# Optimization experiments

Hardware: AMD Instinct MI355X
Metric: run time of the kernel (lower is better)

The kernel has to match this reference:

```python
import jax, jax.numpy as jnp
import numpy as np

N = 20000
E = 320000
HID = 256
NUM_RBF = 32
CUTOFF = 6.0
NUM_EDGE_TYPES = 2
LIGAND_NODE = 1
EPS = 1e-5

CENTERS = jnp.linspace(0.0, CUTOFF, NUM_RBF)  # [R]
GAMMA = 1.0 / max(float(CENTERS[1] - CENTERS[0]) ** 2, 1e-6)


def setup_inputs() -> dict:
    key = jax.random.key(0)
    ks = jax.random.split(key, 16)
    d = {}
    d['h'] = jax.random.normal(ks[0], (N, HID), dtype=jnp.float32)
    d['pos'] = jax.random.normal(ks[1], (N, 3), dtype=jnp.float32)
    d['edge_index'] = jax.random.randint(ks[2], (2, E), 0, N)
    d['edge_type'] = jax.random.randint(ks[3], (E,), 0, NUM_EDGE_TYPES)
    d['node_type'] = jax.random.randint(ks[4], (N,), 0, 2)
    s_in = 1.0 / np.sqrt(3 * HID + NUM_RBF)
    s_h = 1.0 / np.sqrt(HID)
    s_2h = 1.0 / np.sqrt(2 * HID)
    d['emb'] = jax.random.normal(ks[5], (NUM_EDGE_TYPES, HID), dtype=jnp.float32)
    d['W1m'] = jax.random.normal(ks[6], (3 * HID + NUM_RBF, HID), dtype=jnp.float32) * s_in
    d['b1m'] = jnp.zeros((HID,), dtype=jnp.float32)
    d['W2m'] = jax.random.normal(ks[7], (HID, HID), dtype=jnp.float32) * s_h
    d['b2m'] = jnp.zeros((HID,), dtype=jnp.float32)
    d['W1u'] = jax.random.normal(ks[8], (2 * HID, HID), dtype=jnp.float32) * s_2h
    d['b1u'] = jnp.zeros((HID,), dtype=jnp.float32)
    d['W2u'] = jax.random.normal(ks[9], (HID, HID), dtype=jnp.float32) * s_h
    d['b2u'] = jnp.zeros((HID,), dtype=jnp.float32)
    d['ln_g'] = jnp.ones((HID,), dtype=jnp.float32)
    d['ln_b'] = jnp.zeros((HID,), dtype=jnp.float32)
    return d


def _layernorm(x, g, b):
    mu = jnp.mean(x, axis=-1, keepdims=True)
    var = jnp.mean(jnp.square(x - mu), axis=-1, keepdims=True)
    return (x - mu) * jax.lax.rsqrt(var + EPS) * g + b


def reference(h, pos, edge_index, edge_type, node_type,
              emb, W1m, b1m, W2m, b2m, W1u, b1u, W2u, b2u, ln_g, ln_b):
    src, dst = edge_index[0], edge_index[1]
    rel = pos[src] - pos[dst]                      # [E,3]
    dist = jnp.linalg.norm(rel, axis=-1)           # [E]
    radial = jnp.exp(-GAMMA * jnp.square(dist[:, None] - CENTERS[None, :]))  # [E,R]
    edge_kind = emb[edge_type]                     # [E,H]
    m_in = jnp.concatenate([h[src], h[dst], edge_kind, radial], axis=-1)  # [E,3H+R]
    m = jax.nn.silu(m_in @ W1m + b1m)
    m_ij = jax.nn.silu(m @ W2m + b2m)              # [E,H] (dropout = identity in eval)
    seg_sum = jax.ops.segment_sum(m_ij, dst, num_segments=N)               # [N,H]
    cnt = jax.ops.segment_sum(jnp.ones((m_ij.shape[0],), m_ij.dtype), dst, num_segments=N)
    m_i = seg_sum / jnp.maximum(cnt, 1.0)[:, None]
    u = jax.nn.silu(jnp.concatenate([h, m_i], axis=-1) @ W1u + b1u)
    upd = u @ W2u + b2u                            # [N,H]
    lig = (node_type == LIGAND_NODE)[:, None]
    out = jnp.where(lig, _layernorm(h + upd, ln_g, ln_b), h)
    return out
```

## Files before the change

kernel.cpp:

```cpp
#include <hip/hip_runtime.h>
#include <hip/hip_fp16.h>
#include <math.h>

#define NN   20000
#define EE   320000
#define HID  256
#define GAMMA_C ((31.0f/6.0f)*(31.0f/6.0f))

typedef __attribute__((ext_vector_type(8)))  short    short8;
typedef __attribute__((ext_vector_type(8)))  _Float16 half8;
typedef __attribute__((ext_vector_type(16))) float    f32x16;

__device__ __forceinline__ float silu_f(float x) {
    return x / (1.0f + __expf(-x));
}

__device__ __forceinline__ short bf_hi(float x) {
    unsigned u = __float_as_uint(x);
    return (short)((u + 0x7fffu + ((u >> 16) & 1u)) >> 16);
}
__device__ __forceinline__ float bf_tof(short b) {
    return __uint_as_float(((unsigned)(unsigned short)b) << 16);
}
__device__ __forceinline__ void cvt_bf16_pair(float x, short* hi, short* lo) {
    short h = bf_hi(x);
    *hi = h;
    *lo = bf_hi(x - bf_tof(h));
}
__device__ __forceinline__ void cvt_f16_pair(float x, short* hi, short* lo) {
    __half h = __float2half_rn(x);
    *hi = (short)__half_as_ushort(h);
    *lo = (short)__half_as_ushort(__float2half_rn(x - __half2float(h)));
}
__device__ __forceinline__ short f16_bits(float x) {
    return (short)__half_as_ushort(__float2half_rn(x));
}

typedef __attribute__((address_space(1))) const void GV;
typedef __attribute__((address_space(3))) void LV;
__device__ __forceinline__ void gll16(const void* g, void* l) {
    __builtin_amdgcn_global_load_lds((GV*)g, (LV*)l, 16, 0, 0);
}

__device__ __forceinline__ short8 ldsfrag(const short* t, int row, int sg) {
    int s = sg ^ (row & 7);
    return *(const short8*)&t[row * 64 + s * 8];
}
__device__ __forceinline__ half8 ldsfragh32(const short* t, int row, int sg) {
    int s = sg ^ (row & 3);
    return *(const half8*)&t[row * 32 + s * 8];
}
__device__ __forceinline__ short8 ldsfrag32(const short* t, int row, int sg) {
    int s = sg ^ (row & 3);
    return *(const short8*)&t[row * 32 + s * 8];
}
__device__ __forceinline__ half8 ldsfragh(const short* t, int row, int sg) {
    int s = sg ^ (row & 7);
    return *(const half8*)&t[row * 64 + s * 8];
}

#define S0 (NN*HID)
#define S1 (2*HID)
#define S2 (256*800)
#define S3 (256*256)
#define S4 (256*512)
#define S5 (256*256)
#define PREP_TOTAL (S0+S1+S2+S3+S4+S5)

__global__ __launch_bounds__(256) void prep_all(
    const float* __restrict__ h, const float* __restrict__ emb,
    const float* __restrict__ W1m, const float* __restrict__ W2m,
    const float* __restrict__ W1u, const float* __restrict__ W2u,
    short* __restrict__ hpl, short* __restrict__ embpl,
    short* __restrict__ w1t, short* __restrict__ w2t,
    short* __restrict__ w1ut, short* __restrict__ w2ut)
{
    int i = blockIdx.x * 256 + threadIdx.x;
    float x; short *hi, *lo; int o; int f16 = 0;
    if (i < S0)              { x = h[i];   hi = hpl;   lo = hpl + S0;   o = i; }
    else if ((i -= S0) < S1) { x = emb[i]; hi = embpl; lo = embpl + S1; o = i; }
    else if ((i -= S1) < S2) { int n = i / 800, k = i - n * 800;
                               x = W1m[k * 256 + n]; hi = w1t; lo = w1t + S2; o = i; }
    else if ((i -= S2) < S3) { int n = i >> 8, k = i & 255;
                               x = W2m[k * 256 + n]; hi = w2t; lo = w2t + S3; o = i; f16 = 1; }
    else if ((i -= S3) < S4) { int n = i >> 9, k = i & 511;
                               x = W1u[k * 256 + n]; hi = w1ut; lo = w1ut + S4; o = i; }
    else if ((i -= S4) < S5) { int n = i >> 8, k = i & 255;
                               x = W2u[k * 256 + n]; hi = w2ut; lo = w2ut + S5; o = i; f16 = 1; }
    else return;
    short hb, lb;
    if (f16) cvt_f16_pair(x, &hb, &lb); else cvt_bf16_pair(x, &hb, &lb);
    hi[o] = hb; lo[o] = lb;
}

__global__ __launch_bounds__(512, 4) void edge_mlp1(
    const short* __restrict__ hpl, const short* __restrict__ embpl,
    const short* __restrict__ w1t, const float* __restrict__ b1,
    const float* __restrict__ pos, const int* __restrict__ ei,
    const int* __restrict__ etype,
    short* __restrict__ mhi, float* __restrict__ cnt)
{
    __shared__ __align__(16) short At[2][128 * 64];
    __shared__ __align__(16) short Bt[2][128 * 64];
    __shared__ int srcS[128], dstS[128], etS[128];
    __shared__ float distS[128];

    const int tid = threadIdx.x, l = tid & 63, w = tid >> 6;
    const int e0 = blockIdx.x * 128;
    const int cb = blockIdx.y;
    const int mh = w >> 2, ns = w & 3;

    if (tid < 128) {
        int s = ei[e0 + tid], d = ei[EE + e0 + tid];
        srcS[tid] = s; dstS[tid] = d; etS[tid] = etype[e0 + tid];
        float dx = pos[3*s]   - pos[3*d];
        float dy = pos[3*s+1] - pos[3*d+1];
        float dz = pos[3*s+2] - pos[3*d+2];
        distS[tid] = sqrtf(dx*dx + dy*dy + dz*dz);
        if (cb == 0) atomicAdd(&cnt[d], 1.0f);
    }
    __syncthreads();

    auto stageA = [&](int buf, int c) {
        if (c < 24) {
            #pragma unroll
            for (int jj = 0; jj < 2; ++jj) {
                int j = w * 2 + jj;
                int row = j * 8 + (l >> 3), s = l & 7;
                int sg = s ^ (row & 7);
                int hl = sg >> 2, q = sg & 3;
                const short* gp;
                if (c < 8)
                    gp = hpl + (size_t)hl * (NN*HID) + (size_t)srcS[row] * HID + c*32 + q*8;
                else if (c < 16)
                    gp = hpl + (size_t)hl * (NN*HID) + (size_t)dstS[row] * HID + (c-8)*32 + q*8;
                else
                    gp = embpl + hl * (2*HID) + etS[row] * HID + (c-16)*32 + q*8;
                gll16(gp, &At[buf][j * 512]);
            }
        } else {
            #pragma unroll
            for (int jj = 0; jj < 2; ++jj) {
                int it = tid * 2 + jj;
                int row = it >> 3, s = it & 7;
                int sg = s ^ (row & 7);
                int hl = sg >> 2, q = sg & 3;
                float d = distS[row];
                short8 v;
                #pragma unroll
                for (int k8 = 0; k8 < 8; ++k8) {
                    float cen = (float)(q * 8 + k8) * (6.0f / 31.0f);
                    float t = d - cen;
                    float f = __expf(-GAMMA_C * t * t);
                    short hb = bf_hi(f);
                    v[k8] = hl ? bf_hi(f - bf_tof(hb)) : hb;
                }
                *(short8*)&At[buf][row * 64 + s * 8] = v;
            }
        }
    };
    auto stageB = [&](int buf, int c) {
        #pragma unroll
        for (int jj = 0; jj < 2; ++jj) {
            int j = w * 2 + jj;
            int n = j * 8 + (l >> 3), s = l & 7;
            int sg = s ^ (n & 7);
            int hl = sg >> 2, q = sg & 3;
            const short* gp = w1t + (size_t)hl * (256*800)
                            + (size_t)(cb*128 + n) * 800 + c*32 + q*8;
            gll16(gp, &Bt[buf][j * 512]);
        }
    };

    f32x16 acc[2];
    #pragma unroll
    for (int a = 0; a < 2; ++a)
        #pragma unroll
        for (int q = 0; q < 16; ++q) acc[a][q] = 0.0f;

    stageA(0, 0); stageB(0, 0);
    __syncthreads();

    int cur = 0;
    for (int c = 0; c < 25; ++c) {
        if (c < 24) { stageA(cur ^ 1, c + 1); stageB(cur ^ 1, c + 1); }
        #pragma unroll
        for (int t2 = 0; t2 < 2; ++t2) {
            short8 aF[2][2], bF[2];
            #pragma unroll
            for (int mf = 0; mf < 2; ++mf) {
                int row = mh * 64 + mf * 32 + (l & 31);
                #pragma unroll
                for (int hl = 0; hl < 2; ++hl)
                    aF[mf][hl] = ldsfrag(&At[cur][0], row, hl * 4 + t2 * 2 + (l >> 5));
            }
            {
                int n = ns * 32 + (l & 31);
                #pragma unroll
                for (int hl = 0; hl < 2; ++hl)
                    bF[hl] = ldsfrag(&Bt[cur][0], n, hl * 4 + t2 * 2 + (l >> 5));
            }
            #pragma unroll
            for (int mf = 0; mf < 2; ++mf) {
                acc[mf] = __builtin_amdgcn_mfma_f32_32x32x16_bf16(aF[mf][0], bF[0], acc[mf], 0, 0, 0);
                acc[mf] = __builtin_amdgcn_mfma_f32_32x32x16_bf16(aF[mf][0], bF[1], acc[mf], 0, 0, 0);
                acc[mf] = __builtin_amdgcn_mfma_f32_32x32x16_bf16(aF[mf][1], bF[0], acc[mf], 0, 0, 0);
            }
        }
        __syncthreads();
        cur ^= 1;
    }

    {
        int col = cb * 128 + ns * 32 + (l & 31);
        float bb = b1[col];
        #pragma unroll
        for (int mf = 0; mf < 2; ++mf)
            #pragma unroll
            for (int r = 0; r < 16; ++r) {
                int row = mh * 64 + mf * 32 + (r & 3) + 8 * (r >> 2) + 4 * (l >> 5);
                float v = silu_f(acc[mf][r] + bb);
                mhi[(size_t)(e0 + row) * HID + col] = f16_bits(v);
            }
    }
}

__global__ __launch_bounds__(512, 4) void edge_mlp2(
    const short* __restrict__ mhi, const short* __restrict__ w2t,
    const float* __restrict__ b2, const int* __restrict__ ei,
    float* __restrict__ seg)
{
    __shared__ __align__(16) short Ah[2][128 * 32];
    __shared__ __align__(16) short Bh[2][128 * 32];
    __shared__ __align__(16) short Bl[2][128 * 32];
    __shared__ int dstS[128];
    const int tid = threadIdx.x, l = tid & 63, w = tid >> 6;
    const int e0 = blockIdx.x * 128;
    const int cb = blockIdx.y;
    const int mh = w >> 2, ns = w & 3;
    if (tid < 128) dstS[tid] = ei[EE + e0 + tid];
    __syncthreads();

    auto stageA = [&](int buf, int c) {
        int row = w * 16 + (l >> 2), s = l & 3;
        int sg = s ^ (row & 3);
        gll16(mhi + (size_t)(e0 + row) * HID + c * 32 + sg * 8, &Ah[buf][w * 512]);
    };
    auto stageB = [&](int buf, int c) {
        #pragma unroll
        for (int jj = 0; jj < 2; ++jj) {
            int j = w * 2 + jj;
            int hf = j >> 3, jn = j & 7;
            int n = jn * 16 + (l >> 2), s = l & 3;
            int sg = s ^ (n & 3);
            const short* gp = w2t + (size_t)hf * (256*256)
                            + (size_t)(cb*128 + n) * HID + c * 32 + sg * 8;
            gll16(gp, hf ? &Bl[buf][jn * 512] : &Bh[buf][jn * 512]);
        }
    };

    f32x16 acc[2];
    #pragma unroll
    for (int a = 0; a < 2; ++a)
        #pragma unroll
        for (int q = 0; q < 16; ++q) acc[a][q] = 0.0f;

    stageA(0, 0); stageB(0, 0);
    __syncthreads();

    int cur = 0;
    for (int c = 0; c < 8; ++c) {
        if (c < 7) { stageA(cur ^ 1, c + 1); stageB(cur ^ 1, c + 1); }
        #pragma unroll
        for (int t2 = 0; t2 < 2; ++t2) {
            int sg = t2 * 2 + (l >> 5);
            half8 aF[2], bH, bL;
            #pragma unroll
            for (int mf = 0; mf < 2; ++mf)
                aF[mf] = ldsfragh32(&Ah[cur][0], mh * 64 + mf * 32 + (l & 31), sg);
            {
                int n = ns * 32 + (l & 31);
                bH = ldsfragh32(&Bh[cur][0], n, sg);
                bL = ldsfragh32(&Bl[cur][0], n, sg);
            }
            #pragma unroll
            for (int mf = 0; mf < 2; ++mf) {
                acc[mf] = __builtin_amdgcn_mfma_f32_32x32x16_f16(aF[mf], bH, acc[mf], 0, 0, 0);
                acc[mf] = __builtin_amdgcn_mfma_f32_32x32x16_f16(aF[mf], bL, acc[mf], 0, 0, 0);
            }
        }
        __syncthreads();
        cur ^= 1;
    }

    {
        int col = cb * 128 + ns * 32 + (l & 31);
        float bb = b2[col];
        #pragma unroll
        for (int mf = 0; mf < 2; ++mf)
            #pragma unroll
            for (int r = 0; r < 16; ++r) {
                int row = mh * 64 + mf * 32 + (r & 3) + 8 * (r >> 2) + 4 * (l >> 5);
                float v = silu_f(acc[mf][r] + bb);
                atomicAdd(&seg[(size_t)dstS[row] * HID + col], v);
            }
    }
}

__global__ __launch_bounds__(256) void mi_prep(
    const float* __restrict__ seg, const float* __restrict__ cnt,
    short* __restrict__ mipl)
{
    int i = blockIdx.x * 256 + threadIdx.x;
    int row = i >> 8;
    float v = seg[i] / fmaxf(cnt[row], 1.0f);
    short hb, lb;
    cvt_bf16_pair(v, &hb, &lb);
    mipl[i] = hb;
    mipl[(size_t)NN * HID + i] = lb;
}

__global__ __launch_bounds__(512) void node_mlp1(
    const short* __restrict__ hpl, const short* __restrict__ mipl,
    const short* __restrict__ w1ut, const float* __restrict__ b1,
    short* __restrict__ u)
{
    __shared__ __align__(16) short At[128 * 64];
    __shared__ __align__(16) short Bt[256 * 64];
    const int tid = threadIdx.x, l = tid & 63, w = tid >> 6;
    const int n0 = blockIdx.x * 128;
    const int mh = w >> 2, ns = w & 3;

    f32x16 acc[2][2];
    #pragma unroll
    for (int a = 0; a < 2; ++a)
        #pragma unroll
        for (int b = 0; b < 2; ++b)
            #pragma unroll
            for (int q = 0; q < 16; ++q) acc[a][b][q] = 0.0f;

    for (int c = 0; c < 16; ++c) {
        #pragma unroll
        for (int jj = 0; jj < 2; ++jj) {
            int j = w * 2 + jj;
            int row = j * 8 + (l >> 3), s = l & 7;
            int sg = s ^ (row & 7);
            int hl = sg >> 2, q = sg & 3;
            int node = min(n0 + row, NN - 1);
            const short* gp = (c < 8)
                ? hpl  + (size_t)hl * (NN*HID) + (size_t)node * HID + c * 32 + q * 8
                : mipl + (size_t)hl * (NN*HID) + (size_t)node * HID + (c - 8) * 32 + q * 8;
            gll16(gp, &At[j * 512]);
        }
        #pragma unroll
        for (int jj = 0; jj < 4; ++jj) {
            int j = w * 4 + jj;
            int n = j * 8 + (l >> 3), s = l & 7;
            int sg = s ^ (n & 7);
            int hl = sg >> 2, q = sg & 3;
            const short* gp = w1ut + (size_t)hl * (256*512) + n * 512 + c * 32 + q * 8;
            gll16(gp, &Bt[j * 512]);
        }
        __syncthreads();
        #pragma unroll
        for (int t2 = 0; t2 < 2; ++t2) {
            short8 aF[2][2], bF[2][2];
            #pragma unroll
            for (int mf = 0; mf < 2; ++mf) {
                int row = mh * 64 + mf * 32 + (l & 31);
                #pragma unroll
                for (int hl = 0; hl < 2; ++hl)
                    aF[mf][hl] = ldsfrag(At, row, hl * 4 + t2 * 2 + (l >> 5));
            }
            #pragma unroll
            for (int nf = 0; nf < 2; ++nf) {
                int n = ns * 64 + nf * 32 + (l & 31);
                #pragma unroll
                for (int hl = 0; hl < 2; ++hl)
                    bF[nf][hl] = ldsfrag(Bt, n, hl * 4 + t2 * 2 + (l >> 5));
            }
            #pragma unroll
            for (int mf = 0; mf < 2; ++mf)
                #pragma unroll
                for (int nf = 0; nf < 2; ++nf) {
                    acc[mf][nf] = __builtin_amdgcn_mfma_f32_32x32x16_bf16(aF[mf][0], bF[nf][0], acc[mf][nf], 0, 0, 0);
                    acc[mf][nf] = __builtin_amdgcn_mfma_f32_32x32x16_bf16(aF[mf][0], bF[nf][1], acc[mf][nf], 0, 0, 0);
                    acc[mf][nf] = __builtin_amdgcn_mfma_f32_32x32x16_bf16(aF[mf][1], bF[nf][0], acc[mf][nf], 0, 0, 0);
                }
        }
        __syncthreads();
    }
    #pragma unroll
    for (int nf = 0; nf < 2; ++nf) {
        int col = ns * 64 + nf * 32 + (l & 31);
        float bb = b1[col];
        #pragma unroll
        for (int mf = 0; mf < 2; ++mf)
            #pragma unroll
            for (int r = 0; r < 16; ++r) {
                int row = mh * 64 + mf * 32 + (r & 3) + 8 * (r >> 2) + 4 * (l >> 5);
                if (n0 + row < NN) {
                    float v = silu_f(acc[mf][nf][r] + bb);
                    u[(size_t)(n0 + row) * HID + col] = f16_bits(v);
                }
            }
    }
}

__global__ __launch_bounds__(512) void node_mlp2(
    const short* __restrict__ u, const short* __restrict__ w2ut,
    const float* __restrict__ b2, const float* __restrict__ h,
    const int* __restrict__ ntype, const float* __restrict__ lng,
    const float* __restrict__ lnb, float* __restrict__ out)
{
    __shared__ __align__(16) short Ah[128 * 64];
    __shared__ __align__(16) short Bh[256 * 64];
    __shared__ __align__(16) short Bl[256 * 64];
    __shared__ float red1[4][128], red2[4][128];
    __shared__ float muS[128], rsS[128];
    const int tid = threadIdx.x, l = tid & 63, w = tid >> 6;
    const int n0 = blockIdx.x * 128;
    const int mh = w >> 2, ns = w & 3;

    f32x16 acc[2][2];
    #pragma unroll
    for (int a = 0; a < 2; ++a)
        #pragma unroll
        for (int b = 0; b < 2; ++b)
            #pragma unroll
            for (int q = 0; q < 16; ++q) acc[a][b][q] = 0.0f;

    for (int c = 0; c < 4; ++c) {
        #pragma unroll
        for (int jj = 0; jj < 2; ++jj) {
            int j = w * 2 + jj;
            int row = j * 8 + (l >> 3), s = l & 7;
            int sg = s ^ (row & 7);
            int node = min(n0 + row, NN - 1);
            gll16(u + (size_t)node * HID + c * 64 + sg * 8, &Ah[j * 512]);
        }
        #pragma unroll
        for (int jj = 0; jj < 8; ++jj) {
            int j = w * 8 + jj;
            int hf = j >> 5;
            int n = (j & 31) * 8 + (l >> 3), s = l & 7;
            int sg = s ^ (n & 7);
            const short* gp = w2ut + (size_t)hf * (256*256) + n * HID + c * 64 + sg * 8;
            gll16(gp, hf ? &Bl[(j & 31) * 512] : &Bh[(j & 31) * 512]);
        }
        __syncthreads();
        #pragma unroll
        for (int t2 = 0; t2 < 4; ++t2) {
            int sg = t2 * 2 + (l >> 5);
            half8 aF[2], bH[2], bL[2];
            #pragma unroll
            for (int mf = 0; mf < 2; ++mf)
                aF[mf] = ldsfragh(Ah, mh * 64 + mf * 32 + (l & 31), sg);
            #pragma unroll
            for (int nf = 0; nf < 2; ++nf) {
                int n = ns * 64 + nf * 32 + (l & 31);
                bH[nf] = ldsfragh(Bh, n, sg);
                bL[nf] = ldsfragh(Bl, n, sg);
            }
            #pragma unroll
            for (int mf = 0; mf < 2; ++mf)
                #pragma unroll
                for (int nf = 0; nf < 2; ++nf) {
                    acc[mf][nf] = __builtin_amdgcn_mfma_f32_32x32x16_f16(aF[mf], bH[nf], acc[mf][nf], 0, 0, 0);
                    acc[mf][nf] = __builtin_amdgcn_mfma_f32_32x32x16_f16(aF[mf], bL[nf], acc[mf][nf], 0, 0, 0);
                }
        }
        __syncthreads();
    }

    #pragma unroll
    for (int nf = 0; nf < 2; ++nf) {
        int col = ns * 64 + nf * 32 + (l & 31);
        float bb = b2[col];
        #pragma unroll
        for (int mf = 0; mf < 2; ++mf)
            #pragma unroll
            for (int r = 0; r < 16; ++r) {
                int row = mh * 64 + mf * 32 + (r & 3) + 8 * (r >> 2) + 4 * (l >> 5);
                int node = min(n0 + row, NN - 1);
                acc[mf][nf][r] += bb + h[(size_t)node * HID + col];
            }
    }
    #pragma unroll
    for (int mf = 0; mf < 2; ++mf)
        #pragma unroll
        for (int r = 0; r < 16; ++r) {
            float v1 = acc[mf][0][r] + acc[mf][1][r];
            float v2 = acc[mf][0][r]*acc[mf][0][r] + acc[mf][1][r]*acc[mf][1][r];
            #pragma unroll
            for (int off = 16; off >= 1; off >>= 1) {
                v1 += __shfl_xor(v1, off, 64);
                v2 += __shfl_xor(v2, off, 64);
            }
            if ((l & 31) == 0) {
                int row = mh * 64 + mf * 32 + (r & 3) + 8 * (r >> 2) + 4 * (l >> 5);
                red1[ns][row] = v1; red2[ns][row] = v2;
            }
        }
    __syncthreads();
    if (tid < 128) {
        float s1 = red1[0][tid] + red1[1][tid] + red1[2][tid] + red1[3][tid];
        float s2 = red2[0][tid] + red2[1][tid] + red2[2][tid] + red2[3][tid];
        float mu = s1 * (1.0f / 256.0f);
        float var = s2 * (1.0f / 256.0f) - mu * mu;
        muS[tid] = mu;
        rsS[tid] = rsqrtf(var + 1e-5f);
    }
    __syncthreads();
    #pragma unroll
    for (int nf = 0; nf < 2; ++nf) {
        int col = ns * 64 + nf * 32 + (l & 31);
        float g = lng[col], bt = lnb[col];
        #pragma unroll
        for (int mf = 0; mf < 2; ++mf)
            #pragma unroll
            for (int r = 0; r < 16; ++r) {
                int row = mh * 64 + mf * 32 + (r & 3) + 8 * (r >> 2) + 4 * (l >> 5);
                int node = n0 + row;
                if (node < NN) {
                    float y;
                    if (ntype[node] == 1)
                        y = (acc[mf][nf][r] - muS[row]) * rsS[row] * g + bt;
                    else
                        y = h[(size_t)node * HID + col];
                    out[(size_t)node * HID + col] = y;
                }
            }
    }
}

#define SWZ(k, e) ((e) ^ ((((k) >> 2) & 7) << 2))

__global__ __launch_bounds__(256) void edge_fp32(
    const float* __restrict__ h, const float* __restrict__ pos,
    const int* __restrict__ ei, const int* __restrict__ etype,
    const float* __restrict__ emb,
    const float* __restrict__ W1, const float* __restrict__ b1,
    const float* __restrict__ W2, const float* __restrict__ b2,
    float* __restrict__ seg, float* __restrict__ cnt)
{
    __shared__ float A1T[16][32];
    __shared__ float Bt[16][256];
    __shared__ float A2T[256][32];
    __shared__ float distS[32];
    __shared__ int   srcS[32], dstS[32], etS[32];
    const int tid = threadIdx.x;
    const int e0  = blockIdx.x * 32;
    if (tid < 32) {
        const int e = e0 + tid;
        const int s = ei[e];
        const int d = ei[EE + e];
        srcS[tid] = s; dstS[tid] = d; etS[tid] = etype[e];
        const float dx = pos[3*s+0] - pos[3*d+0];
        const float dy = pos[3*s+1] - pos[3*d+1];
        const float dz = pos[3*s+2] - pos[3*d+2];
        distS[tid] = sqrtf(dx*dx + dy*dy + dz*dz);
        atomicAdd(&cnt[d], 1.0f);
    }
    __syncthreads();
    const int c0 = (tid & 63) * 4;
    const int r0 = (tid >> 6) * 8;
    float acc[8][4];
    #pragma unroll
    for (int i = 0; i < 8; ++i)
        #pragma unroll
        for (int j = 0; j < 4; ++j) acc[i][j] = 0.0f;
    const float step  = 6.0f / 31.0f;
    for (int k0 = 0; k0 < 800; k0 += 16) {
        if (tid < 128) {
            const int e = tid >> 2;
            const int q = (tid & 3) * 4;
            const int k = k0 + q;
            float4 v;
            if (k < 256)       v = *(const float4*)&h[(size_t)srcS[e]*HID + k];
            else if (k < 512)  v = *(const float4*)&h[(size_t)dstS[e]*HID + (k - 256)];
            else if (k < 768)  v = *(const float4*)&emb[(size_t)etS[e]*HID + (k - 512)];
            else {
                const float de = distS[e];
                const float t0 = de - step*(float)(k-768);
                const float t1 = de - step*(float)(k-767);
                const float t2 = de - step*(float)(k-766);
                const float t3 = de - step*(float)(k-765);
                v = make_float4(__expf(-GAMMA_C*t0*t0), __expf(-GAMMA_C*t1*t1),
                                __expf(-GAMMA_C*t2*t2), __expf(-GAMMA_C*t3*t3));
            }
            A1T[q+0][e] = v.x; A1T[q+1][e] = v.y;
            A1T[q+2][e] = v.z; A1T[q+3][e] = v.w;
        }
        #pragma unroll
        for (int p = 0; p < 4; ++p) {
            const int idx = p*256 + tid;
            const int k   = idx >> 6;
            const int n   = (idx & 63) * 4;
            *(float4*)&Bt[k][n] = *(const float4*)&W1[(size_t)(k0+k)*HID + n];
        }
        __syncthreads();
        #pragma unroll
        for (int kk = 0; kk < 16; ++kk) {
            const float4 b  = *(const float4*)&Bt[kk][c0];
            const float4 a0 = *(const float4*)&A1T[kk][r0];
            const float4 a1 = *(const float4*)&A1T[kk][r0+4];
            const float a[8] = {a0.x,a0.y,a0.z,a0.w,a1.x,a1.y,a1.z,a1.w};
            #pragma unroll
            for (int i = 0; i < 8; ++i) {
                acc[i][0] = fmaf(a[i], b.x, acc[i][0]);
                acc[i][1] = fmaf(a[i], b.y, acc[i][1]);
                acc[i][2] = fmaf(a[i], b.z, acc[i][2]);
                acc[i][3] = fmaf(a[i], b.w, acc[i][3]);
            }
        }
        __syncthreads();
    }
    {
        const float4 b1v = *(const float4*)&b1[c0];
        const float bb[4] = {b1v.x, b1v.y, b1v.z, b1v.w};
        #pragma unroll
        for (int j = 0; j < 4; ++j) {
            const int k = c0 + j;
            #pragma unroll
            for (int i = 0; i < 8; ++i) {
                const float x = acc[i][j] + bb[j];
                A2T[k][SWZ(k, r0+i)] = silu_f(x);
                acc[i][j] = 0.0f;
            }
        }
    }
    __syncthreads();
    for (int k0 = 0; k0 < HID; k0 += 16) {
        #pragma unroll
        for (int p = 0; p < 4; ++p) {
            const int idx = p*256 + tid;
            const int k   = idx >> 6;
            const int n   = (idx & 63) * 4;
            *(float4*)&Bt[k][n] = *(const float4*)&W2[(size_t)(k0+k)*HID + n];
        }
        __syncthreads();
        #pragma unroll
        for (int kk = 0; kk < 16; ++kk) {
            const int K = k0 + kk;
            const float4 b  = *(const float4*)&Bt[kk][c0];
            const float4 a0 = *(const float4*)&A2T[K][SWZ(K, r0)];
            const float4 a1 = *(const float4*)&A2T[K][SWZ(K, r0+4)];
            const float a[8] = {a0.x,a0.y,a0.z,a0.w,a1.x,a1.y,a1.z,a1.w};
            #pragma unroll
            for (int i = 0; i < 8; ++i) {
                acc[i][0] = fmaf(a[i], b.x, acc[i][0]);
                acc[i][1] = fmaf(a[i], b.y, acc[i][1]);
                acc[i][2] = fmaf(a[i], b.z, acc[i][2]);
                acc[i][3] = fmaf(a[i], b.w, acc[i][3]);
            }
        }
        __syncthreads();
    }
    {
        const float4 b2v = *(const float4*)&b2[c0];
        const float bb[4] = {b2v.x, b2v.y, b2v.z, b2v.w};
        #pragma unroll
        for (int i = 0; i < 8; ++i) {
            const int d = dstS[r0 + i];
            float* outp = &seg[(size_t)d*HID + c0];
            #pragma unroll
            for (int j = 0; j < 4; ++j) {
                const float x = acc[i][j] + bb[j];
                atomicAdd(&outp[j], silu_f(x));
            }
        }
    }
}

__global__ __launch_bounds__(256) void node_fp32(
    const float* __restrict__ h, const float* __restrict__ seg,
    const float* __restrict__ cnt, const int* __restrict__ ntype,
    const float* __restrict__ W1, const float* __restrict__ b1,
    const float* __restrict__ W2, const float* __restrict__ b2,
    const float* __restrict__ lng, const float* __restrict__ lnb,
    float* __restrict__ out)
{
    __shared__ float A1T[16][32];
    __shared__ float Bt[16][256];
    __shared__ float A2T[256][32];
    __shared__ float invS[32];
    const int tid = threadIdx.x;
    const int n0  = blockIdx.x * 32;
    if (tid < 32) invS[tid] = 1.0f / fmaxf(cnt[n0 + tid], 1.0f);
    __syncthreads();
    const int c0 = (tid & 63) * 4;
    const int r0 = (tid >> 6) * 8;
    float acc[8][4];
    #pragma unroll
    for (int i = 0; i < 8; ++i)
        #pragma unroll
        for (int j = 0; j < 4; ++j) acc[i][j] = 0.0f;
    for (int k0 = 0; k0 < 512; k0 += 16) {
        if (tid < 128) {
            const int e = tid >> 2;
            const int q = (tid & 3) * 4;
            const int k = k0 + q;
            float4 v;
            if (k < 256) v = *(const float4*)&h[(size_t)(n0+e)*HID + k];
            else {
                v = *(const float4*)&seg[(size_t)(n0+e)*HID + (k - 256)];
                const float ic = invS[e];
                v.x *= ic; v.y *= ic; v.z *= ic; v.w *= ic;
            }
            A1T[q+0][e] = v.x; A1T[q+1][e] = v.y;
            A1T[q+2][e] = v.z; A1T[q+3][e] = v.w;
        }
        #pragma unroll
        for (int p = 0; p < 4; ++p) {
            const int idx = p*256 + tid;
            const int k   = idx >> 6;
            const int n   = (idx & 63) * 4;
            *(float4*)&Bt[k][n] = *(const float4*)&W1[(size_t)(k0+k)*HID + n];
        }
        __syncthreads();
        #pragma unroll
        for (int kk = 0; kk < 16; ++kk) {
            const float4 b  = *(const float4*)&Bt[kk][c0];
            const float4 a0 = *(const float4*)&A1T[kk][r0];
            const float4 a1 = *(const float4*)&A1T[kk][r0+4];
            const float a[8] = {a0.x,a0.y,a0.z,a0.w,a1.x,a1.y,a1.z,a1.w};
            #pragma unroll
            for (int i = 0; i < 8; ++i) {
                acc[i][0] = fmaf(a[i], b.x, acc[i][0]);
                acc[i][1] = fmaf(a[i], b.y, acc[i][1]);
                acc[i][2] = fmaf(a[i], b.z, acc[i][2]);
                acc[i][3] = fmaf(a[i], b.w, acc[i][3]);
            }
        }
        __syncthreads();
    }
    {
        const float4 b1v = *(const float4*)&b1[c0];
        const float bb[4] = {b1v.x, b1v.y, b1v.z, b1v.w};
        #pragma unroll
        for (int j = 0; j < 4; ++j) {
            const int k = c0 + j;
            #pragma unroll
            for (int i = 0; i < 8; ++i) {
                const float x = acc[i][j] + bb[j];
                A2T[k][SWZ(k, r0+i)] = silu_f(x);
                acc[i][j] = 0.0f;
            }
        }
    }
    __syncthreads();
    for (int k0 = 0; k0 < HID; k0 += 16) {
        #pragma unroll
        for (int p = 0; p < 4; ++p) {
            const int idx = p*256 + tid;
            const int k   = idx >> 6;
            const int n   = (idx & 63) * 4;
            *(float4*)&Bt[k][n] = *(const float4*)&W2[(size_t)(k0+k)*HID + n];
        }
        __syncthreads();
        #pragma unroll
        for (int kk = 0; kk < 16; ++kk) {
            const int K = k0 + kk;
            const float4 b  = *(const float4*)&Bt[kk][c0];
            const float4 a0 = *(const float4*)&A2T[K][SWZ(K, r0)];
            const float4 a1 = *(const float4*)&A2T[K][SWZ(K, r0+4)];
            const float a[8] = {a0.x,a0.y,a0.z,a0.w,a1.x,a1.y,a1.z,a1.w};
            #pragma unroll
            for (int i = 0; i < 8; ++i) {
                acc[i][0] = fmaf(a[i], b.x, acc[i][0]);
                acc[i][1] = fmaf(a[i], b.y, acc[i][1]);
                acc[i][2] = fmaf(a[i], b.z, acc[i][2]);
                acc[i][3] = fmaf(a[i], b.w, acc[i][3]);
            }
        }
        __syncthreads();
    }
    {
        const float4 b2v = *(const float4*)&b2[c0];
        const float bb[4] = {b2v.x, b2v.y, b2v.z, b2v.w};
        float4 hv[8];
        #pragma unroll
        for (int i = 0; i < 8; ++i) {
            hv[i] = *(const float4*)&h[(size_t)(n0+r0+i)*HID + c0];
            acc[i][0] = hv[i].x + acc[i][0] + bb[0];
            acc[i][1] = hv[i].y + acc[i][1] + bb[1];
            acc[i][2] = hv[i].z + acc[i][2] + bb[2];
            acc[i][3] = hv[i].w + acc[i][3] + bb[3];
        }
        float s1[8], s2[8];
        #pragma unroll
        for (int i = 0; i < 8; ++i) {
            s1[i] = acc[i][0] + acc[i][1] + acc[i][2] + acc[i][3];
            s2[i] = acc[i][0]*acc[i][0] + acc[i][1]*acc[i][1]
                  + acc[i][2]*acc[i][2] + acc[i][3]*acc[i][3];
        }
        #pragma unroll
        for (int off = 32; off >= 1; off >>= 1) {
            #pragma unroll
            for (int i = 0; i < 8; ++i) {
                s1[i] += __shfl_xor(s1[i], off, 64);
                s2[i] += __shfl_xor(s2[i], off, 64);
            }
        }
        const float4 gv = *(const float4*)&lng[c0];
        const float4 bv = *(const float4*)&lnb[c0];
        const float g[4] = {gv.x, gv.y, gv.z, gv.w};
        const float bb2[4] = {bv.x, bv.y, bv.z, bv.w};
        #pragma unroll
        for (int i = 0; i < 8; ++i) {
            const int n = n0 + r0 + i;
            const bool lig = (ntype[n] == 1);
            float4 y;
            if (lig) {
                const float mu  = s1[i] * (1.0f/256.0f);
                const float var = s2[i] * (1.0f/256.0f) - mu*mu;
                const float rs  = rsqrtf(var + 1e-5f);
                y.x = (acc[i][0] - mu) * rs * g[0] + bb2[0];
                y.y = (acc[i][1] - mu) * rs * g[1] + bb2[1];
                y.z = (acc[i][2] - mu) * rs * g[2] + bb2[2];
                y.w = (acc[i][3] - mu) * rs * g[3] + bb2[3];
            } else {
                y = hv[i];
            }
            *(float4*)&out[(size_t)n*HID + c0] = y;
        }
    }
}

extern "C" void kernel_launch(void* const* d_in, const int* in_sizes, int n_in,
                              void* d_out, int out_size, void* d_ws, size_t ws_size,
                              hipStream_t stream) {
    (void)in_sizes; (void)n_in; (void)out_size;
    const float* h    = (const float*)d_in[0];
    const float* pos  = (const float*)d_in[1];
    const int*   ei   = (const int*)  d_in[2];
    const int*   et   = (const int*)  d_in[3];
    const int*   nt   = (const int*)  d_in[4];
    const float* emb  = (const float*)d_in[5];
    const float* W1m  = (const float*)d_in[6];
    const float* b1m  = (const float*)d_in[7];
    const float* W2m  = (const float*)d_in[8];
    const float* b2m  = (const float*)d_in[9];
    const float* W1u  = (const float*)d_in[10];
    const float* b1u  = (const float*)d_in[11];
    const float* W2u  = (const float*)d_in[12];
    const float* b2u  = (const float*)d_in[13];
    const float* lng  = (const float*)d_in[14];
    const float* lnb  = (const float*)d_in[15];
    float* out = (float*)d_out;

    size_t o = 0;
    auto al = [&](size_t b) { size_t r = o; o = (o + b + 511) & ~(size_t)511; return r; };
    const size_t o_seg  = al((size_t)NN * HID * 4);
    const size_t o_cnt  = al((size_t)NN * 4);
    const size_t o_zend = o;
    const size_t o_hpl  = al((size_t)2 * NN * HID * 2);
    const size_t o_emb  = al((size_t)2 * 2 * HID * 2);
    const size_t o_w1t  = al((size_t)2 * 256 * 800 * 2);
    const size_t o_w2t  = al((size_t)2 * 256 * 256 * 2);
    const size_t o_w1ut = al((size_t)2 * 256 * 512 * 2);
    const size_t o_w2ut = al((size_t)2 * 256 * 256 * 2);
    const size_t o_mipl = al((size_t)2 * NN * HID * 2);
    const size_t o_upl  = al((size_t)NN * HID * 2);
    const size_t o_mhi  = al((size_t)EE * HID * 2);
    const size_t need = o;

    char* ws = (char*)d_ws;
    float* seg = (float*)(ws + o_seg);
    float* cnt = (float*)(ws + o_cnt);

    if (ws_size >= need) {
        short* hpl   = (short*)(ws + o_hpl);
        short* embpl = (short*)(ws + o_emb);
        short* w1t   = (short*)(ws + o_w1t);
        short* w2t   = (short*)(ws + o_w2t);
        short* w1ut  = (short*)(ws + o_w1ut);
        short* w2ut  = (short*)(ws + o_w2ut);
        short* mipl  = (short*)(ws + o_mipl);
        short* upl   = (short*)(ws + o_upl);
        short* mhi   = (short*)(ws + o_mhi);

        hipMemsetAsync(d_ws, 0, o_zend, stream);
        prep_all<<<PREP_TOTAL / 256, 256, 0, stream>>>(
            h, emb, W1m, W2m, W1u, W2u, hpl, embpl, w1t, w2t, w1ut, w2ut);
        edge_mlp1<<<dim3(EE / 128, 2), 512, 0, stream>>>(
            hpl, embpl, w1t, b1m, pos, ei, et, mhi, cnt);
        edge_mlp2<<<dim3(EE / 128, 2), 512, 0, stream>>>(mhi, w2t, b2m, ei, seg);
        mi_prep<<<(NN * HID) / 256, 256, 0, stream>>>(seg, cnt, mipl);
        const int nb = (NN + 127) / 128;
        node_mlp1<<<nb, 512, 0, stream>>>(hpl, mipl, w1ut, b1u, upl);
        node_mlp2<<<nb, 512, 0, stream>>>(upl, w2ut, b2u, h, nt, lng, lnb, out);
    } else {
        hipMemsetAsync(d_ws, 0, ((size_t)NN * HID + NN) * sizeof(float), stream);
        float* seg0 = (float*)d_ws;
        float* cnt0 = seg0 + (size_t)NN * HID;
        edge_fp32<<<EE / 32, 256, 0, stream>>>(h, pos, ei, et, emb,
                                               W1m, b1m, W2m, b2m, seg0, cnt0);
        node_fp32<<<NN / 32, 256, 0, stream>>>(h, seg0, cnt0, nt,
                                               W1u, b1u, W2u, b2u, lng, lnb, out);
    }
}
```

Measured before the change: 935.8 us.

## Fold edge-type embedding into per-type bias table and enlarge edge_mlp1 tile

Since the edge-type embedding takes one of only two values, its product with W1m plus b1m is precomputed into a 2x256 table by a small kernel and added in the epilogue, which shrinks the K dimension of the first edge GEMM from 800 to 544. edge_mlp1 is also retiled to 256 edges by the full 256 output columns per block, which removes the two-column-block grid and the duplicated gathers of h rows. The mainloop becomes a hand-pipelined double buffer with explicit vmcnt waits and raw barriers. The cost is more accumulator registers and LDS per block (occupancy bound lowered to 2) and a serial single-block tprep launch.

Result: faster. 872.4 us (-6.8%).

```diff
diff --git a/kernel.cpp b/kernel.cpp
--- a/kernel.cpp
+++ b/kernel.cpp
@@ -5,6 +5,7 @@
 #define NN   20000
 #define EE   320000
 #define HID  256
+#define K1P  544
 #define GAMMA_C ((31.0f/6.0f)*(31.0f/6.0f))
 
 typedef __attribute__((ext_vector_type(8)))  short    short8;
@@ -50,10 +51,6 @@
     int s = sg ^ (row & 3);
     return *(const half8*)&t[row * 32 + s * 8];
 }
-__device__ __forceinline__ short8 ldsfrag32(const short* t, int row, int sg) {
-    int s = sg ^ (row & 3);
-    return *(const short8*)&t[row * 32 + s * 8];
-}
 __device__ __forceinline__ half8 ldsfragh(const short* t, int row, int sg) {
     int s = sg ^ (row & 7);
     return *(const half8*)&t[row * 64 + s * 8];
@@ -61,7 +58,7 @@
 
 #define S0 (NN*HID)
 #define S1 (2*HID)
-#define S2 (256*800)
+#define S2 (256*544)
 #define S3 (256*256)
 #define S4 (256*512)
 #define S5 (256*256)
@@ -79,8 +76,9 @@
     float x; short *hi, *lo; int o; int f16 = 0;
     if (i < S0)              { x = h[i];   hi = hpl;   lo = hpl + S0;   o = i; }
     else if ((i -= S0) < S1) { x = emb[i]; hi = embpl; lo = embpl + S1; o = i; }
-    else if ((i -= S1) < S2) { int n = i / 800, k = i - n * 800;
-                               x = W1m[k * 256 + n]; hi = w1t; lo = w1t + S2; o = i; }
+    else if ((i -= S1) < S2) { int n = i / 544, k = i - n * 544;
+                               int ok = (k < 512) ? k : (k + 256);
+                               x = W1m[ok * 256 + n]; hi = w1t; lo = w1t + S2; o = i; }
     else if ((i -= S2) < S3) { int n = i >> 8, k = i & 255;
                                x = W2m[k * 256 + n]; hi = w2t; lo = w2t + S3; o = i; f16 = 1; }
     else if ((i -= S3) < S4) { int n = i >> 9, k = i & 511;
@@ -93,55 +91,68 @@
     hi[o] = hb; lo[o] = lb;
 }
 
-__global__ __launch_bounds__(512, 4) void edge_mlp1(
-    const short* __restrict__ hpl, const short* __restrict__ embpl,
-    const short* __restrict__ w1t, const float* __restrict__ b1,
-    const float* __restrict__ pos, const int* __restrict__ ei,
-    const int* __restrict__ etype,
+__global__ __launch_bounds__(512) void tprep(
+    const float* __restrict__ W1m, const float* __restrict__ b1,
+    const float* __restrict__ emb, float* __restrict__ T)
+{
+    int tid = threadIdx.x;
+    int e = tid >> 8, n = tid & 255;
+    float s = b1[n];
+    for (int k = 0; k < 256; ++k)
+        s += emb[e * 256 + k] * W1m[(512 + k) * 256 + n];
+    T[e * 256 + n] = s;
+}
+
+__global__ __launch_bounds__(512, 2) void edge_mlp1(
+    const short* __restrict__ hpl, const short* __restrict__ w1t,
+    const float* __restrict__ Ttab, const float* __restrict__ pos,
+    const int* __restrict__ ei, const int* __restrict__ etype,
     short* __restrict__ mhi, float* __restrict__ cnt)
 {
-    __shared__ __align__(16) short At[2][128 * 64];
-    __shared__ __align__(16) short Bt[2][128 * 64];
-    __shared__ int srcS[128], dstS[128], etS[128];
-    __shared__ float distS[128];
+    __shared__ __align__(16) short At[2][256 * 64];
+    __shared__ __align__(16) short Bt[2][256 * 64];
+    __shared__ int srcS[256], dstS[256], etS[256];
+    __shared__ float distS[256];
 
     const int tid = threadIdx.x, l = tid & 63, w = tid >> 6;
-    const int e0 = blockIdx.x * 128;
-    const int cb = blockIdx.y;
+    const int e0 = blockIdx.x * 256;
     const int mh = w >> 2, ns = w & 3;
 
-    if (tid < 128) {
+    if (tid < 256) {
         int s = ei[e0 + tid], d = ei[EE + e0 + tid];
         srcS[tid] = s; dstS[tid] = d; etS[tid] = etype[e0 + tid];
         float dx = pos[3*s]   - pos[3*d];
         float dy = pos[3*s+1] - pos[3*d+1];
         float dz = pos[3*s+2] - pos[3*d+2];
         distS[tid] = sqrtf(dx*dx + dy*dy + dz*dz);
-        if (cb == 0) atomicAdd(&cnt[d], 1.0f);
+        atomicAdd(&cnt[d], 1.0f);
     }
     __syncthreads();
 
-    auto stageA = [&](int buf, int c) {
-        if (c < 24) {
-            #pragma unroll
-            for (int jj = 0; jj < 2; ++jj) {
-                int j = w * 2 + jj;
-                int row = j * 8 + (l >> 3), s = l & 7;
-                int sg = s ^ (row & 7);
-                int hl = sg >> 2, q = sg & 3;
-                const short* gp;
-                if (c < 8)
-                    gp = hpl + (size_t)hl * (NN*HID) + (size_t)srcS[row] * HID + c*32 + q*8;
-                else if (c < 16)
-                    gp = hpl + (size_t)hl * (NN*HID) + (size_t)dstS[row] * HID + (c-8)*32 + q*8;
-                else
-                    gp = embpl + hl * (2*HID) + etS[row] * HID + (c-16)*32 + q*8;
-                gll16(gp, &At[buf][j * 512]);
+    unsigned offS[4], offD[4], offB[4];
+    #pragma unroll
+    for (int jj = 0; jj < 4; ++jj) {
+        int j = w * 4 + jj;
+        int row = j * 8 + (l >> 3), s = l & 7;
+        int sg = s ^ (row & 7);
+        int hl = sg >> 2, q = sg & 3;
+        offS[jj] = (unsigned)hl * (NN*HID) + (unsigned)srcS[row] * HID + q*8;
+        offD[jj] = (unsigned)hl * (NN*HID) + (unsigned)dstS[row] * HID + q*8;
+        offB[jj] = (unsigned)hl * (256*544) + (unsigned)row * 544 + q*8;
+    }
+
+    auto stage = [&](int buf, int c) {
+        if (c < 16) {
+            #pragma unroll
+            for (int jj = 0; jj < 4; ++jj) {
+                const short* gp = (c < 8) ? (hpl + offS[jj] + c*32)
+                                          : (hpl + offD[jj] + (c-8)*32);
+                gll16(gp, &At[buf][(w*4 + jj) * 512]);
             }
         } else {
             #pragma unroll
-            for (int jj = 0; jj < 2; ++jj) {
-                int it = tid * 2 + jj;
+            for (int jj = 0; jj < 4; ++jj) {
+                int it = tid * 4 + jj;
                 int row = it >> 3, s = it & 7;
                 int sg = s ^ (row & 7);
                 int hl = sg >> 2, q = sg & 3;
@@ -157,69 +168,70 @@
                 }
                 *(short8*)&At[buf][row * 64 + s * 8] = v;
             }
-        }
+            asm volatile("s_waitcnt lgkmcnt(0)" ::: "memory");
+        }
+        #pragma unroll
+        for (int jj = 0; jj < 4; ++jj)
+            gll16(w1t + offB[jj] + c*32, &Bt[buf][(w*4 + jj) * 512]);
     };
-    auto stageB = [&](int buf, int c) {
-        #pragma unroll
-        for (int jj = 0; jj < 2; ++jj) {
-            int j = w * 2 + jj;
-            int n = j * 8 + (l >> 3), s = l & 7;
-            int sg = s ^ (n & 7);
-            int hl = sg >> 2, q = sg & 3;
-            const short* gp = w1t + (size_t)hl * (256*800)
-                            + (size_t)(cb*128 + n) * 800 + c*32 + q*8;
-            gll16(gp, &Bt[buf][j * 512]);
-        }
-    };
-
-    f32x16 acc[2];
-    #pragma unroll
-    for (int a = 0; a < 2; ++a)
-        #pragma unroll
-        for (int q = 0; q < 16; ++q) acc[a][q] = 0.0f;
-
-    stageA(0, 0); stageB(0, 0);
-    __syncthreads();
-
-    int cur = 0;
-    for (int c = 0; c < 25; ++c) {
-        if (c < 24) { stageA(cur ^ 1, c + 1); stageB(cur ^ 1, c + 1); }
+
+    f32x16 acc[4][2];
+    #pragma unroll
+    for (int a = 0; a < 4; ++a)
+        #pragma unroll
+        for (int b = 0; b < 2; ++b)
+            #pragma unroll
+            for (int q = 0; q < 16; ++q) acc[a][b][q] = 0.0f;
+
+    stage(0, 0);
+    stage(1, 1);
+
+    for (int c = 0; c <= 16; ++c) {
+        if (c <= 14)      asm volatile("s_waitcnt vmcnt(8)" ::: "memory");
+        else if (c == 15) asm volatile("s_waitcnt vmcnt(4)" ::: "memory");
+        else              asm volatile("s_waitcnt vmcnt(0)" ::: "memory");
+        __builtin_amdgcn_s_barrier();
+        __builtin_amdgcn_sched_barrier(0);
+
+        const int buf = c & 1;
         #pragma unroll
         for (int t2 = 0; t2 < 2; ++t2) {
-            short8 aF[2][2], bF[2];
-            #pragma unroll
-            for (int mf = 0; mf < 2; ++mf) {
-                int row = mh * 64 + mf * 32 + (l & 31);
+            short8 bF[2][2];
+            #pragma unroll
+            for (int nf = 0; nf < 2; ++nf)
                 #pragma unroll
                 for (int hl = 0; hl < 2; ++hl)
-                    aF[mf][hl] = ldsfrag(&At[cur][0], row, hl * 4 + t2 * 2 + (l >> 5));
-            }
-            {
-                int n = ns * 32 + (l & 31);
+                    bF[nf][hl] = ldsfrag(&Bt[buf][0], ns*64 + nf*32 + (l & 31),
+                                         hl*4 + t2*2 + (l >> 5));
+            #pragma unroll
+            for (int mf = 0; mf < 4; ++mf) {
+                int arow = mh*128 + mf*32 + (l & 31);
+                short8 aF0 = ldsfrag(&At[buf][0], arow, 0*4 + t2*2 + (l >> 5));
+                short8 aF1 = ldsfrag(&At[buf][0], arow, 1*4 + t2*2 + (l >> 5));
                 #pragma unroll
-                for (int hl = 0; hl < 2; ++hl)
-                    bF[hl] = ldsfrag(&Bt[cur][0], n, hl * 4 + t2 * 2 + (l >> 5));
-            }
-            #pragma unroll
-            for (int mf = 0; mf < 2; ++mf) {
-                acc[mf] = __builtin_amdgcn_mfma_f32_32x32x16_bf16(aF[mf][0], bF[0], acc[mf], 0, 0, 0);
-                acc[mf] = __builtin_amdgcn_mfma_f32_32x32x16_bf16(aF[mf][0], bF[1], acc[mf], 0, 0, 0);
-                acc[mf] = __builtin_amdgcn_mfma_f32_32x32x16_bf16(aF[mf][1], bF[0], acc[mf], 0, 0, 0);
-            }
-        }
-        __syncthreads();
-        cur ^= 1;
-    }
-
-    {
-        int col = cb * 128 + ns * 32 + (l & 31);
-        float bb = b1[col];
-        #pragma unroll
-        for (int mf = 0; mf < 2; ++mf)
+                for (int nf = 0; nf < 2; ++nf) {
+                    acc[mf][nf] = __builtin_amdgcn_mfma_f32_32x32x16_bf16(aF0, bF[nf][0], acc[mf][nf], 0, 0, 0);
+                    acc[mf][nf] = __builtin_amdgcn_mfma_f32_32x32x16_bf16(aF0, bF[nf][1], acc[mf][nf], 0, 0, 0);
+                    acc[mf][nf] = __builtin_amdgcn_mfma_f32_32x32x16_bf16(aF1, bF[nf][0], acc[mf][nf], 0, 0, 0);
+                }
+            }
+        }
+
+        __builtin_amdgcn_sched_barrier(0);
+        __builtin_amdgcn_s_barrier();
+        if (c + 2 <= 16) stage(buf, c + 2);
+    }
+
+    #pragma unroll
+    for (int nf = 0; nf < 2; ++nf) {
+        int col = ns*64 + nf*32 + (l & 31);
+        #pragma unroll
+        for (int mf = 0; mf < 4; ++mf)
             #pragma unroll
             for (int r = 0; r < 16; ++r) {
-                int row = mh * 64 + mf * 32 + (r & 3) + 8 * (r >> 2) + 4 * (l >> 5);
-                float v = silu_f(acc[mf][r] + bb);
+                int row = mh*128 + mf*32 + (r & 3) + 8*(r >> 2) + 4*(l >> 5);
+                float tv = Ttab[etS[row] * 256 + col];
+                float v = silu_f(acc[mf][nf][r] + tv);
                 mhi[(size_t)(e0 + row) * HID + col] = f16_bits(v);
             }
     }
@@ -857,10 +869,11 @@
     const size_t o_zend = o;
     const size_t o_hpl  = al((size_t)2 * NN * HID * 2);
     const size_t o_emb  = al((size_t)2 * 2 * HID * 2);
-    const size_t o_w1t  = al((size_t)2 * 256 * 800 * 2);
+    const size_t o_w1t  = al((size_t)2 * 256 * 544 * 2);
     const size_t o_w2t  = al((size_t)2 * 256 * 256 * 2);
     const size_t o_w1ut = al((size_t)2 * 256 * 512 * 2);
     const size_t o_w2ut = al((size_t)2 * 256 * 256 * 2);
+    const size_t o_T    = al((size_t)2 * 256 * 4);
     const size_t o_mipl = al((size_t)2 * NN * HID * 2);
     const size_t o_upl  = al((size_t)NN * HID * 2);
     const size_t o_mhi  = al((size_t)EE * HID * 2);
@@ -877,6 +890,7 @@
         short* w2t   = (short*)(ws + o_w2t);
         short* w1ut  = (short*)(ws + o_w1ut);
         short* w2ut  = (short*)(ws + o_w2ut);
+        float* T     = (float*)(ws + o_T);
         short* mipl  = (short*)(ws + o_mipl);
         short* upl   = (short*)(ws + o_upl);
         short* mhi   = (short*)(ws + o_mhi);
@@ -884,8 +898,9 @@
         hipMemsetAsync(d_ws, 0, o_zend, stream);
         prep_all<<<PREP_TOTAL / 256, 256, 0, stream>>>(
             h, emb, W1m, W2m, W1u, W2u, hpl, embpl, w1t, w2t, w1ut, w2ut);
-        edge_mlp1<<<dim3(EE / 128, 2), 512, 0, stream>>>(
-            hpl, embpl, w1t, b1m, pos, ei, et, mhi, cnt);
+        tprep<<<1, 512, 0, stream>>>(W1m, b1m, emb, T);
+        edge_mlp1<<<EE / 256, 512, 0, stream>>>(
+            hpl, w1t, T, pos, ei, et, mhi, cnt);
         edge_mlp2<<<dim3(EE / 128, 2), 512, 0, stream>>>(mhi, w2t, b2m, ei, seg);
         mi_prep<<<(NN * HID) / 256, 256, 0, stream>>>(seg, cnt, mipl);
         const int nb = (NN + 127) / 128;
```
